# Kernel tuning notes

Measured on AMD Instinct MI355X. Metric: run time of the kernel, lower is better.

## Reference

```python
import jax, jax.numpy as jnp
import numpy as np

N_NODES = 50000
N_EDGES = 400000
HID = 256
NUM_LAYERS = 2
NUM_LEVELS = 8  # depth of the constructed leveled DAG


def _build_dag_edges():
    # Leveled DAG: NUM_LEVELS levels of equal size; every edge goes from
    # level l (src) to level l+1 (dst), guaranteeing termination in
    # exactly NUM_LEVELS topological sweeps.
    rng = np.random.default_rng(0)
    per_level = N_NODES // NUM_LEVELS
    dst_level = rng.integers(1, NUM_LEVELS, size=N_EDGES)
    dst = dst_level * per_level + rng.integers(0, per_level, size=N_EDGES)
    src = (dst_level - 1) * per_level + rng.integers(0, per_level, size=N_EDGES)
    return jnp.asarray(np.stack([src, dst]).astype(np.int32))


def setup_inputs() -> dict:
    key = jax.random.key(0)
    ks = jax.random.split(key, 8)
    s = 0.05
    V = jax.random.normal(ks[0], (N_NODES, HID), dtype=jnp.float32)
    E = _build_dag_edges()
    dense_w = jax.random.normal(ks[1], (HID, HID), dtype=jnp.float32) * s
    dense_b = jax.random.normal(ks[2], (HID,), dtype=jnp.float32) * s
    gru_w_ih = jax.random.normal(ks[3], (NUM_LAYERS, 3 * HID, HID), dtype=jnp.float32) * s
    gru_w_hh = jax.random.normal(ks[4], (NUM_LAYERS, 3 * HID, HID), dtype=jnp.float32) * s
    gru_b_ih = jax.random.normal(ks[5], (NUM_LAYERS, 3 * HID), dtype=jnp.float32) * s
    gru_b_hh = jax.random.normal(ks[6], (NUM_LAYERS, 3 * HID), dtype=jnp.float32) * s
    return {"V": V, "E": E, "dense_w": dense_w, "dense_b": dense_b,
            "gru_w_ih": gru_w_ih, "gru_w_hh": gru_w_hh,
            "gru_b_ih": gru_b_ih, "gru_b_hh": gru_b_hh}


def _gru_cell(x, h, w_ih, w_hh, b_ih, b_hh):
    gi = x @ w_ih.T + b_ih
    gh = h @ w_hh.T + b_hh
    i_r, i_z, i_n = jnp.split(gi, 3, axis=-1)
    h_r, h_z, h_n = jnp.split(gh, 3, axis=-1)
    r = jax.nn.sigmoid(i_r + h_r)
    z = jax.nn.sigmoid(i_z + h_z)
    n = jnp.tanh(i_n + r * h_n)
    return (1.0 - z) * n + z * h


def _dag_gru_layer(x, src, dst, w_ih, w_hh, b_ih, b_hh):
    N = x.shape[0]
    H = w_hh.shape[1]

    def step(carry, _):
        hidden, avail = carry
        # nodes that are dst of an edge whose source is still available
        blocked = jnp.zeros((N,), dtype=bool).at[dst].max(avail[src])
        leaf = avail & ~blocked
        use = leaf[dst]  # edges feeding a leaf node this sweep
        msgs = jnp.where(use[:, None], hidden[src], 0.0)  # [E, H]
        agg = jax.ops.segment_sum(msgs, dst, num_segments=N)  # [N, H]
        new_h = _gru_cell(x, agg, w_ih, w_hh, b_ih, b_hh)
        hidden = jnp.where(leaf[:, None], new_h, hidden)
        return (hidden, avail & ~leaf), None

    init = (jnp.zeros((N, H), dtype=x.dtype), jnp.ones((N,), dtype=bool))
    (hidden, _), _ = jax.lax.scan(step, init, None, length=NUM_LEVELS)
    return hidden


def reference(V, E, dense_w, dense_b, gru_w_ih, gru_w_hh, gru_b_ih, gru_b_hh):
    src, dst = E[0], E[1]
    hidden = V @ dense_w.T + dense_b
    for l in range(NUM_LAYERS):
        hidden = _dag_gru_layer(hidden, src, dst,
                                gru_w_ih[l], gru_w_hh[l],
                                gru_b_ih[l], gru_b_hh[l])
    return hidden
```

## Files before the change

kernel.cpp:

```cpp
#include <hip/hip_runtime.h>

#define HID 256
#define NSTEPS 8

typedef __attribute__((ext_vector_type(4))) float f32x4;
typedef __attribute__((ext_vector_type(8))) short s16x8;

__device__ __forceinline__ unsigned short f2bf(float f) {
  unsigned u = __builtin_bit_cast(unsigned, f);
  u += 0x7fffu + ((u >> 16) & 1u);
  return (unsigned short)(u >> 16);
}
__device__ __forceinline__ float bf2f(unsigned short s) {
  return __builtin_bit_cast(float, ((unsigned)s) << 16);
}

__device__ __forceinline__ f32x4 mfma16(s16x8 a, s16x8 b, f32x4 c) {
  return __builtin_amdgcn_mfma_f32_16x16x32_bf16(a, b, c, 0, 0, 0);
}

__device__ __forceinline__ void split3(const float* p, s16x8& a0, s16x8& a1, s16x8& a2) {
  f32x4 u = *(const f32x4*)p;
  f32x4 v = *(const f32x4*)(p + 4);
  float f[8] = {u[0], u[1], u[2], u[3], v[0], v[1], v[2], v[3]};
#pragma unroll
  for (int j = 0; j < 8; ++j) {
    unsigned short l0 = f2bf(f[j]);
    float r1 = f[j] - bf2f(l0);
    unsigned short l1 = f2bf(r1);
    float r2 = r1 - bf2f(l1);
    a0[j] = (short)l0;
    a1[j] = (short)l1;
    a2[j] = (short)f2bf(r2);
  }
}


__global__ void k_limb(const float* __restrict__ in, short* __restrict__ o0,
                       short* __restrict__ o1, short* __restrict__ o2, int n) {
  int i = blockIdx.x * 256 + threadIdx.x;
  if (i < n) {
    float x = in[i];
    unsigned short l0 = f2bf(x);
    float r1 = x - bf2f(l0);
    unsigned short l1 = f2bf(r1);
    o0[i] = (short)l0;
    o1[i] = (short)l1;
    o2[i] = (short)f2bf(r1 - bf2f(l1));
  }
}


__global__ void k_indeg(const int* __restrict__ dst, int* __restrict__ indeg, int E) {
  int e = blockIdx.x * blockDim.x + threadIdx.x;
  if (e < E) atomicAdd(&indeg[dst[e]], 1);
}

__global__ void k_blocksum(const int* __restrict__ indeg, int* __restrict__ bsum, int N) {
  __shared__ int s[256];
  int i = blockIdx.x * 256 + threadIdx.x;
  s[threadIdx.x] = (i < N) ? indeg[i] : 0;
  __syncthreads();
  for (int st = 128; st > 0; st >>= 1) {
    if (threadIdx.x < st) s[threadIdx.x] += s[threadIdx.x + st];
    __syncthreads();
  }
  if (threadIdx.x == 0) bsum[blockIdx.x] = s[0];
}

__global__ void k_bscan(const int* __restrict__ bsum, int* __restrict__ boff,
                        int NB, int* __restrict__ total) {
  if (threadIdx.x == 0 && blockIdx.x == 0) {
    int a = 0;
    for (int i = 0; i < NB; ++i) { boff[i] = a; a += bsum[i]; }
    *total = a;
  }
}

__global__ void k_scan3(const int* __restrict__ indeg, const int* __restrict__ boff,
                        int* __restrict__ csr_off, int N) {
  __shared__ int s[256];
  int tx = threadIdx.x;
  int i = blockIdx.x * 256 + tx;
  int v = (i < N) ? indeg[i] : 0;
  s[tx] = v;
  __syncthreads();
  for (int st = 1; st < 256; st <<= 1) {
    int t = (tx >= st) ? s[tx - st] : 0;
    __syncthreads();
    s[tx] += t;
    __syncthreads();
  }
  if (i < N) csr_off[i] = boff[blockIdx.x] + s[tx] - v;
}

__global__ void k_fill(const int* __restrict__ src, const int* __restrict__ dst,
                       const int* __restrict__ csr_off, int* __restrict__ cursor,
                       int* __restrict__ csr_src, int E) {
  int e = blockIdx.x * blockDim.x + threadIdx.x;
  if (e < E) {
    int d = dst[e];
    int p = atomicAdd(&cursor[d], 1);
    csr_src[csr_off[d] + p] = src[e];
  }
}


__global__ void k_aggf(const float* __restrict__ H, int s, int PB,
                       const int* __restrict__ csr_off, const int* __restrict__ csr_src,
                       float* __restrict__ aggF, short* __restrict__ G0,
                       short* __restrict__ G1, short* __restrict__ G2) {
  int c = threadIdx.x;
  for (int r = blockIdx.x; r < PB; r += gridDim.x) {
    int node = s * PB + r;
    int b = csr_off[node], e = csr_off[node + 1];
    float acc = 0.f;
    for (int j = b; j < e; ++j) acc += H[(size_t)csr_src[j] * HID + c];
    size_t o = (size_t)r * HID + c;
    aggF[o] = acc;
    unsigned short l0 = f2bf(acc);
    float r1 = acc - bf2f(l0);
    unsigned short l1 = f2bf(r1);
    G0[o] = (short)l0;
    G1[o] = (short)l1;
    G2[o] = (short)f2bf(r1 - bf2f(l1));
  }
}

__global__ __launch_bounds__(256, 2)
void k_dense8(const float* __restrict__ V, const short* __restrict__ dwS,
              const float* __restrict__ db,
              short* __restrict__ A0, short* __restrict__ A1,
              short* __restrict__ A2, int M) {
  __shared__ s16x8 lds[2][24 * 64];
  const int tid = threadIdx.x;
  const int w = tid >> 6, lane = tid & 63;
  const int lr = lane & 15, lg = lane >> 4;
  const int c0 = blockIdx.x * 128;
  const int m0 = blockIdx.y * 64 + w * 16;
  const float* xrow = V + (size_t)min(m0 + lr, M - 1) * HID;

  const short* sp[6];
  int so[6];
#pragma unroll
  for (int q = 0; q < 6; ++q) {
    int f = w * 6 + q;
    int a = f >> 3, t = f & 7;
    sp[q] = dwS + a * (HID * HID) + (size_t)(c0 + t * 16 + lr) * HID + lg * 8;
    so[q] = f * 64 + lane;
  }

  s16x8 rr[6];
#pragma unroll
  for (int q = 0; q < 6; ++q) rr[q] = *(const s16x8*)(sp[q]);
#pragma unroll
  for (int q = 0; q < 6; ++q) lds[0][so[q]] = rr[q];

  f32x4 acc[8];
#pragma unroll
  for (int t = 0; t < 8; ++t) acc[t] = (f32x4){0.f, 0.f, 0.f, 0.f};

  for (int kc = 0; kc < 8; ++kc) {
    if (kc < 7) {
#pragma unroll
      for (int q = 0; q < 6; ++q) rr[q] = *(const s16x8*)(sp[q] + (kc + 1) * 32);
    }
    __syncthreads();
    const s16x8* buf = lds[kc & 1];
    int kb = kc * 32 + lg * 8;
    s16x8 x0, x1, x2;
    split3(xrow + kb, x0, x1, x2);
#pragma unroll
    for (int t = 0; t < 8; ++t) {
      s16x8 w0f = buf[(0 * 8 + t) * 64 + lane];
      s16x8 w1f = buf[(1 * 8 + t) * 64 + lane];
      s16x8 w2f = buf[(2 * 8 + t) * 64 + lane];
      f32x4 a = acc[t];
      a = mfma16(x0, w0f, a);
      a = mfma16(x0, w1f, a);
      a = mfma16(x1, w0f, a);
      a = mfma16(x1, w1f, a);
      a = mfma16(x0, w2f, a);
      a = mfma16(x2, w0f, a);
      acc[t] = a;
    }
    if (kc < 7) {
#pragma unroll
      for (int q = 0; q < 6; ++q) lds[(kc + 1) & 1][so[q]] = rr[q];
    }
  }

#pragma unroll
  for (int t = 0; t < 8; ++t) {
    int col = c0 + t * 16 + lr;
    float bb = db[col];
#pragma unroll
    for (int r = 0; r < 4; ++r) {
      int row = m0 + lg * 4 + r;
      if (row < M) {
        float v = acc[t][r] + bb;
        unsigned short l0 = f2bf(v);
        float r1 = v - bf2f(l0);
        unsigned short l1 = f2bf(r1);
        size_t o = (size_t)row * HID + col;
        A0[o] = (short)l0;
        A1[o] = (short)l1;
        A2[o] = (short)f2bf(r1 - bf2f(l1));
      }
    }
  }
}

template<bool OUTL>
__global__ __launch_bounds__(256, 2)
void k_step8(const short* __restrict__ X0, const short* __restrict__ X1,
             const short* __restrict__ X2,
             const short* __restrict__ G0, const short* __restrict__ G1,
             const short* __restrict__ G2,
             const float* __restrict__ aggF,
             const short* __restrict__ wSL,
             const float* __restrict__ bi, const float* __restrict__ bh,
             int s, int PB, float* __restrict__ Hf,
             short* __restrict__ L0, short* __restrict__ L1, short* __restrict__ L2) {
  __shared__ s16x8 lds[2][36 * 64];
  const int tid = threadIdx.x;
  const int w = tid >> 6, lane = tid & 63;
  const int lr = lane & 15, lg = lane >> 4;
  const int c0 = blockIdx.x * 32;
  const int m0w = blockIdx.y * 128 + w * 32;
  const int nb = s * PB;
  const int AS = 768 * HID;

  const short* sp[9];
  int so[9];
#pragma unroll
  for (int q = 0; q < 9; ++q) {
    int f = w * 9 + q;
    int a = f / 6, gt = f - a * 6, g = gt >> 1, t = gt & 1;
    sp[q] = wSL + (size_t)a * AS + (size_t)(g * HID + c0 + t * 16 + lr) * HID + lg * 8;
    so[q] = f * 64 + lane;
  }

  s16x8 rr[9];
#pragma unroll
  for (int q = 0; q < 9; ++q) rr[q] = *(const s16x8*)(sp[q]);
#pragma unroll
  for (int q = 0; q < 9; ++q) lds[0][so[q]] = rr[q];

  f32x4 acci[3][2][2], acch[3][2][2];
#pragma unroll
  for (int g = 0; g < 3; ++g)
#pragma unroll
    for (int t = 0; t < 2; ++t)
#pragma unroll
      for (int rg = 0; rg < 2; ++rg) {
        acci[g][t][rg] = (f32x4){0.f, 0.f, 0.f, 0.f};
        acch[g][t][rg] = (f32x4){0.f, 0.f, 0.f, 0.f};
      }

  int rowA[2];
  rowA[0] = min(m0w + lr, PB - 1);
  rowA[1] = min(m0w + 16 + lr, PB - 1);

  for (int kc = 0; kc < 8; ++kc) {
    if (kc < 7) {
#pragma unroll
      for (int q = 0; q < 9; ++q) rr[q] = *(const s16x8*)(sp[q] + (kc + 1) * 32);
    }
    __syncthreads();
    const s16x8* buf = lds[kc & 1];
    const int kb = kc * 32 + lg * 8;
    s16x8 x0[2], x1[2], x2[2], g0[2], g1[2], g2[2];
#pragma unroll
    for (int rg = 0; rg < 2; ++rg) {
      size_t xb = (size_t)(nb + rowA[rg]) * HID + kb;
      x0[rg] = *(const s16x8*)&X0[xb];
      x1[rg] = *(const s16x8*)&X1[xb];
      x2[rg] = *(const s16x8*)&X2[xb];
      size_t gb = (size_t)rowA[rg] * HID + kb;
      g0[rg] = *(const s16x8*)&G0[gb];
      g1[rg] = *(const s16x8*)&G1[gb];
      g2[rg] = *(const s16x8*)&G2[gb];
    }
#pragma unroll
    for (int g = 0; g < 3; ++g) {
#pragma unroll
      for (int t = 0; t < 2; ++t) {
        s16x8 wi0f = buf[(0 * 6 + g * 2 + t) * 64 + lane];
        s16x8 wi1f = buf[(1 * 6 + g * 2 + t) * 64 + lane];
        s16x8 wi2f = buf[(2 * 6 + g * 2 + t) * 64 + lane];
        s16x8 wh0f = buf[(3 * 6 + g * 2 + t) * 64 + lane];
        s16x8 wh1f = buf[(4 * 6 + g * 2 + t) * 64 + lane];
        s16x8 wh2f = buf[(5 * 6 + g * 2 + t) * 64 + lane];
#pragma unroll
        for (int rg = 0; rg < 2; ++rg) {
          f32x4 a = acci[g][t][rg];
          a = mfma16(x0[rg], wi0f, a);
          a = mfma16(x0[rg], wi1f, a);
          a = mfma16(x1[rg], wi0f, a);
          a = mfma16(x1[rg], wi1f, a);
          a = mfma16(x0[rg], wi2f, a);
          a = mfma16(x2[rg], wi0f, a);
          acci[g][t][rg] = a;
          f32x4 h = acch[g][t][rg];
          h = mfma16(g0[rg], wh0f, h);
          h = mfma16(g0[rg], wh1f, h);
          h = mfma16(g1[rg], wh0f, h);
          h = mfma16(g1[rg], wh1f, h);
          h = mfma16(g0[rg], wh2f, h);
          h = mfma16(g2[rg], wh0f, h);
          acch[g][t][rg] = h;
        }
      }
    }
    if (kc < 7) {
#pragma unroll
      for (int q = 0; q < 9; ++q) lds[(kc + 1) & 1][so[q]] = rr[q];
    }
  }

#pragma unroll
  for (int t = 0; t < 2; ++t) {
    int col = c0 + t * 16 + lr;
    float bir = bi[col], biz = bi[HID + col], bin = bi[2 * HID + col];
    float bhr = bh[col], bhz = bh[HID + col], bhn = bh[2 * HID + col];
#pragma unroll
    for (int rg = 0; rg < 2; ++rg) {
#pragma unroll
      for (int r = 0; r < 4; ++r) {
        int row = m0w + rg * 16 + lg * 4 + r;
        if (row < PB) {
          float ir = acci[0][t][rg][r] + bir;
          float iz = acci[1][t][rg][r] + biz;
          float in_ = acci[2][t][rg][r] + bin;
          float hr = acch[0][t][rg][r] + bhr;
          float hz = acch[1][t][rg][r] + bhz;
          float hn = acch[2][t][rg][r] + bhn;
          float rgate = 1.f / (1.f + expf(-(ir + hr)));
          float zg = 1.f / (1.f + expf(-(iz + hz)));
          float ng = tanhf(in_ + rgate * hn);
          float a = aggF[(size_t)row * HID + col];
          float h = (1.f - zg) * ng + zg * a;
          size_t o = (size_t)(nb + row) * HID + col;
          Hf[o] = h;
          if (OUTL) {
            unsigned short l0 = f2bf(h);
            float r1 = h - bf2f(l0);
            unsigned short l1 = f2bf(r1);
            L0[o] = (short)l0;
            L1[o] = (short)l1;
            L2[o] = (short)f2bf(r1 - bf2f(l1));
          }
        }
      }
    }
  }
}


extern "C" void kernel_launch(void* const* d_in, const int* in_sizes, int n_in,
                              void* d_out, int out_size, void* d_ws, size_t ws_size,
                              hipStream_t stream) {
  const float* V = (const float*)d_in[0];
  const int* E = (const int*)d_in[1];
  const float* dense_w = (const float*)d_in[2];
  const float* dense_b = (const float*)d_in[3];
  const float* w_ih = (const float*)d_in[4];
  const float* w_hh = (const float*)d_in[5];
  const float* b_ih = (const float*)d_in[6];
  const float* b_hh = (const float*)d_in[7];
  const int N = in_sizes[0] / HID;
  const int Ecnt = in_sizes[1] / 2;
  const int PB = N / NSTEPS;
  const int* src = E;
  const int* dst = E + Ecnt;
  float* out = (float*)d_out;

  const size_t AS = (size_t)768 * HID;

  char* p = (char*)d_ws;
  short* A0 = (short*)p;   p += (size_t)N * HID * 2;
  short* A1 = (short*)p;   p += (size_t)N * HID * 2;
  short* A2 = (short*)p;   p += (size_t)N * HID * 2;
  float* B = (float*)p;    p += (size_t)N * HID * 4;
  short* B0 = (short*)p;   p += (size_t)N * HID * 2;
  short* B1 = (short*)p;   p += (size_t)N * HID * 2;
  short* B2 = (short*)p;   p += (size_t)N * HID * 2;
  float* aggF = (float*)p; p += (size_t)PB * HID * 4;
  short* G0 = (short*)p;   p += (size_t)PB * HID * 2;
  short* G1 = (short*)p;   p += (size_t)PB * HID * 2;
  short* G2 = (short*)p;   p += (size_t)PB * HID * 2;
  short* dwS = (short*)p;  p += (size_t)3 * HID * HID * 2;
  short* wS = (short*)p;   p += (size_t)2 * 6 * AS * 2;
  int* indeg = (int*)p;    p += (size_t)N * 4;
  int* cursor = (int*)p;   p += (size_t)N * 4;
  int* csr_off = (int*)p;  p += (size_t)(N + 1) * 4;
  int* csr_src = (int*)p;  p += (size_t)Ecnt * 4;
  int* bsum = (int*)p;     p += 256 * 4;
  int* boff = (int*)p;     p += 256 * 4;

  hipMemsetAsync(indeg, 0, (size_t)2 * N * 4, stream);

  const int TB = 256;
  const int egrid = (Ecnt + TB - 1) / TB;
  const int NB = (N + 255) / 256;
  const int wgrid = ((int)AS + 255) / 256;

  k_limb<<<(HID * HID + 255) / 256, TB, 0, stream>>>(
      dense_w, dwS, dwS + HID * HID, dwS + 2 * HID * HID, HID * HID);
  for (int l = 0; l < 2; ++l) {
    k_limb<<<wgrid, TB, 0, stream>>>(w_ih + l * AS, wS + (l * 6 + 0) * AS,
                                     wS + (l * 6 + 1) * AS, wS + (l * 6 + 2) * AS, (int)AS);
    k_limb<<<wgrid, TB, 0, stream>>>(w_hh + l * AS, wS + (l * 6 + 3) * AS,
                                     wS + (l * 6 + 4) * AS, wS + (l * 6 + 5) * AS, (int)AS);
  }

  k_dense8<<<dim3(2, (N + 63) / 64), TB, 0, stream>>>(V, dwS, dense_b, A0, A1, A2, N);

  k_indeg<<<egrid, TB, 0, stream>>>(dst, indeg, Ecnt);
  k_blocksum<<<NB, TB, 0, stream>>>(indeg, bsum, N);
  k_bscan<<<1, 1, 0, stream>>>(bsum, boff, NB, csr_off + N);
  k_scan3<<<NB, TB, 0, stream>>>(indeg, boff, csr_off, N);
  k_fill<<<egrid, TB, 0, stream>>>(src, dst, csr_off, cursor, csr_src, Ecnt);

  const dim3 sgrid(HID / 32, (PB + 127) / 128);

  for (int s = 0; s < NSTEPS; ++s) {
    k_aggf<<<2048, TB, 0, stream>>>(B, s, PB, csr_off, csr_src, aggF, G0, G1, G2);
    k_step8<true><<<sgrid, TB, 0, stream>>>(A0, A1, A2, G0, G1, G2, aggF,
                                            wS, b_ih, b_hh, s, PB, B, B0, B1, B2);
  }
  for (int s = 0; s < NSTEPS; ++s) {
    k_aggf<<<2048, TB, 0, stream>>>(out, s, PB, csr_off, csr_src, aggF, G0, G1, G2);
    k_step8<false><<<sgrid, TB, 0, stream>>>(B0, B1, B2, G0, G1, G2, aggF,
                                             wS + 6 * AS, b_ih + 768, b_hh + 768, s, PB,
                                             out, nullptr, nullptr, nullptr);
  }
}
```

Baseline: 1.492 ms.

## Pipeline both GRU layers across levels in shared launches and vectorize aggregation

Runs layer 0 at level t and layer 1 at level t-1 within the same launch via a z grid dimension, halving the number of sequential aggregation/step launches and doubling per-launch parallelism. Aggregation is rewritten to use one wavefront per node with float4 loads instead of one 256-thread block per node. Adds duplicated aggregate buffers and per-block pointer selection; correctness relies on the layer-1 dependency being satisfied by the previous launch.

```diff
diff --git a/kernel.cpp b/kernel.cpp
--- a/kernel.cpp
+++ b/kernel.cpp
@@ -5,6 +5,7 @@
 
 typedef __attribute__((ext_vector_type(4))) float f32x4;
 typedef __attribute__((ext_vector_type(8))) short s16x8;
+typedef __attribute__((ext_vector_type(4))) short s16x4;
 
 __device__ __forceinline__ unsigned short f2bf(float f) {
   unsigned u = __builtin_bit_cast(unsigned, f);
@@ -106,25 +107,49 @@
 }
 
 
-__global__ void k_aggf(const float* __restrict__ H, int s, int PB,
-                       const int* __restrict__ csr_off, const int* __restrict__ csr_src,
-                       float* __restrict__ aggF, short* __restrict__ G0,
-                       short* __restrict__ G1, short* __restrict__ G2) {
-  int c = threadIdx.x;
-  for (int r = blockIdx.x; r < PB; r += gridDim.x) {
-    int node = s * PB + r;
-    int b = csr_off[node], e = csr_off[node + 1];
-    float acc = 0.f;
-    for (int j = b; j < e; ++j) acc += H[(size_t)csr_src[j] * HID + c];
-    size_t o = (size_t)r * HID + c;
-    aggF[o] = acc;
-    unsigned short l0 = f2bf(acc);
-    float r1 = acc - bf2f(l0);
+__global__ void k_aggf2(const float* __restrict__ HA, const float* __restrict__ HB,
+                        int t, int PB,
+                        const int* __restrict__ csr_off, const int* __restrict__ csr_src,
+                        float* __restrict__ aggFA, float* __restrict__ aggFB,
+                        short* __restrict__ GA0, short* __restrict__ GA1,
+                        short* __restrict__ GA2,
+                        short* __restrict__ GB0, short* __restrict__ GB1,
+                        short* __restrict__ GB2) {
+  const int z = blockIdx.z;
+  const int s = t - z;
+  if (s < 0 || s >= NSTEPS) return;
+  const float* H = z ? HB : HA;
+  float* aggF = z ? aggFB : aggFA;
+  short* G0 = z ? GB0 : GA0;
+  short* G1 = z ? GB1 : GA1;
+  short* G2 = z ? GB2 : GA2;
+
+  const int grp = threadIdx.x >> 6, lane = threadIdx.x & 63;
+  const int r = blockIdx.x * 4 + grp;
+  if (r >= PB) return;
+  const int node = s * PB + r;
+  const int b = csr_off[node], e = csr_off[node + 1];
+  const int c4 = lane * 4;
+  f32x4 acc = (f32x4){0.f, 0.f, 0.f, 0.f};
+  for (int j = b; j < e; ++j) {
+    f32x4 v = *(const f32x4*)&H[(size_t)csr_src[j] * HID + c4];
+    acc[0] += v[0]; acc[1] += v[1]; acc[2] += v[2]; acc[3] += v[3];
+  }
+  size_t o = (size_t)r * HID + c4;
+  *(f32x4*)&aggF[o] = acc;
+  s16x4 g0, g1, g2;
+#pragma unroll
+  for (int q = 0; q < 4; ++q) {
+    unsigned short l0 = f2bf(acc[q]);
+    float r1 = acc[q] - bf2f(l0);
     unsigned short l1 = f2bf(r1);
-    G0[o] = (short)l0;
-    G1[o] = (short)l1;
-    G2[o] = (short)f2bf(r1 - bf2f(l1));
-  }
+    g0[q] = (short)l0;
+    g1[q] = (short)l1;
+    g2[q] = (short)f2bf(r1 - bf2f(l1));
+  }
+  *(s16x4*)&G0[o] = g0;
+  *(s16x4*)&G1[o] = g1;
+  *(s16x4*)&G2[o] = g2;
 }
 
 __global__ __launch_bounds__(256, 2)
@@ -211,17 +236,37 @@
   }
 }
 
-template<bool OUTL>
 __global__ __launch_bounds__(256, 2)
-void k_step8(const short* __restrict__ X0, const short* __restrict__ X1,
-             const short* __restrict__ X2,
-             const short* __restrict__ G0, const short* __restrict__ G1,
-             const short* __restrict__ G2,
-             const float* __restrict__ aggF,
-             const short* __restrict__ wSL,
-             const float* __restrict__ bi, const float* __restrict__ bh,
-             int s, int PB, float* __restrict__ Hf,
-             short* __restrict__ L0, short* __restrict__ L1, short* __restrict__ L2) {
+void k_step2(const short* __restrict__ A0, const short* __restrict__ A1,
+             const short* __restrict__ A2,
+             const short* __restrict__ B0, const short* __restrict__ B1,
+             const short* __restrict__ B2,
+             const short* __restrict__ GA0, const short* __restrict__ GA1,
+             const short* __restrict__ GA2,
+             const short* __restrict__ GB0, const short* __restrict__ GB1,
+             const short* __restrict__ GB2,
+             const float* __restrict__ aggFA, const float* __restrict__ aggFB,
+             const short* __restrict__ wS,
+             const float* __restrict__ b_ih, const float* __restrict__ b_hh,
+             int t, int PB, float* __restrict__ Bfp, float* __restrict__ outp) {
+  const int z = blockIdx.z;
+  const int s = t - z;
+  if (s < 0 || s >= NSTEPS) return;
+
+  const short* X0 = z ? B0 : A0;
+  const short* X1 = z ? B1 : A1;
+  const short* X2 = z ? B2 : A2;
+  const short* G0 = z ? GB0 : GA0;
+  const short* G1 = z ? GB1 : GA1;
+  const short* G2 = z ? GB2 : GA2;
+  const float* aggF = z ? aggFB : aggFA;
+  const int AS = 768 * HID;
+  const short* wSL = wS + (size_t)z * 6 * AS;
+  const float* bi = b_ih + z * 768;
+  const float* bh = b_hh + z * 768;
+  float* Hf = z ? outp : Bfp;
+  const bool outl = (z == 0);
+
   __shared__ s16x8 lds[2][36 * 64];
   const int tid = threadIdx.x;
   const int w = tid >> 6, lane = tid & 63;
@@ -229,15 +274,14 @@
   const int c0 = blockIdx.x * 32;
   const int m0w = blockIdx.y * 128 + w * 32;
   const int nb = s * PB;
-  const int AS = 768 * HID;
 
   const short* sp[9];
   int so[9];
 #pragma unroll
   for (int q = 0; q < 9; ++q) {
     int f = w * 9 + q;
-    int a = f / 6, gt = f - a * 6, g = gt >> 1, t = gt & 1;
-    sp[q] = wSL + (size_t)a * AS + (size_t)(g * HID + c0 + t * 16 + lr) * HID + lg * 8;
+    int a = f / 6, gt = f - a * 6, g = gt >> 1, tt = gt & 1;
+    sp[q] = wSL + (size_t)a * AS + (size_t)(g * HID + c0 + tt * 16 + lr) * HID + lg * 8;
     so[q] = f * 64 + lane;
   }
 
@@ -251,11 +295,11 @@
 #pragma unroll
   for (int g = 0; g < 3; ++g)
 #pragma unroll
-    for (int t = 0; t < 2; ++t)
+    for (int tt = 0; tt < 2; ++tt)
 #pragma unroll
       for (int rg = 0; rg < 2; ++rg) {
-        acci[g][t][rg] = (f32x4){0.f, 0.f, 0.f, 0.f};
-        acch[g][t][rg] = (f32x4){0.f, 0.f, 0.f, 0.f};
+        acci[g][tt][rg] = (f32x4){0.f, 0.f, 0.f, 0.f};
+        acch[g][tt][rg] = (f32x4){0.f, 0.f, 0.f, 0.f};
       }
 
   int rowA[2];
@@ -285,31 +329,31 @@
 #pragma unroll
     for (int g = 0; g < 3; ++g) {
 #pragma unroll
-      for (int t = 0; t < 2; ++t) {
-        s16x8 wi0f = buf[(0 * 6 + g * 2 + t) * 64 + lane];
-        s16x8 wi1f = buf[(1 * 6 + g * 2 + t) * 64 + lane];
-        s16x8 wi2f = buf[(2 * 6 + g * 2 + t) * 64 + lane];
-        s16x8 wh0f = buf[(3 * 6 + g * 2 + t) * 64 + lane];
-        s16x8 wh1f = buf[(4 * 6 + g * 2 + t) * 64 + lane];
-        s16x8 wh2f = buf[(5 * 6 + g * 2 + t) * 64 + lane];
+      for (int tt = 0; tt < 2; ++tt) {
+        s16x8 wi0f = buf[(0 * 6 + g * 2 + tt) * 64 + lane];
+        s16x8 wi1f = buf[(1 * 6 + g * 2 + tt) * 64 + lane];
+        s16x8 wi2f = buf[(2 * 6 + g * 2 + tt) * 64 + lane];
+        s16x8 wh0f = buf[(3 * 6 + g * 2 + tt) * 64 + lane];
+        s16x8 wh1f = buf[(4 * 6 + g * 2 + tt) * 64 + lane];
+        s16x8 wh2f = buf[(5 * 6 + g * 2 + tt) * 64 + lane];
 #pragma unroll
         for (int rg = 0; rg < 2; ++rg) {
-          f32x4 a = acci[g][t][rg];
+          f32x4 a = acci[g][tt][rg];
           a = mfma16(x0[rg], wi0f, a);
           a = mfma16(x0[rg], wi1f, a);
           a = mfma16(x1[rg], wi0f, a);
           a = mfma16(x1[rg], wi1f, a);
           a = mfma16(x0[rg], wi2f, a);
           a = mfma16(x2[rg], wi0f, a);
-          acci[g][t][rg] = a;
-          f32x4 h = acch[g][t][rg];
+          acci[g][tt][rg] = a;
+          f32x4 h = acch[g][tt][rg];
           h = mfma16(g0[rg], wh0f, h);
           h = mfma16(g0[rg], wh1f, h);
           h = mfma16(g1[rg], wh0f, h);
           h = mfma16(g1[rg], wh1f, h);
           h = mfma16(g0[rg], wh2f, h);
           h = mfma16(g2[rg], wh0f, h);
-          acch[g][t][rg] = h;
+          acch[g][tt][rg] = h;
         }
       }
     }
@@ -320,8 +364,8 @@
   }
 
 #pragma unroll
-  for (int t = 0; t < 2; ++t) {
-    int col = c0 + t * 16 + lr;
+  for (int tt = 0; tt < 2; ++tt) {
+    int col = c0 + tt * 16 + lr;
     float bir = bi[col], biz = bi[HID + col], bin = bi[2 * HID + col];
     float bhr = bh[col], bhz = bh[HID + col], bhn = bh[2 * HID + col];
 #pragma unroll
@@ -330,12 +374,12 @@
       for (int r = 0; r < 4; ++r) {
         int row = m0w + rg * 16 + lg * 4 + r;
         if (row < PB) {
-          float ir = acci[0][t][rg][r] + bir;
-          float iz = acci[1][t][rg][r] + biz;
-          float in_ = acci[2][t][rg][r] + bin;
-          float hr = acch[0][t][rg][r] + bhr;
-          float hz = acch[1][t][rg][r] + bhz;
-          float hn = acch[2][t][rg][r] + bhn;
+          float ir = acci[0][tt][rg][r] + bir;
+          float iz = acci[1][tt][rg][r] + biz;
+          float in_ = acci[2][tt][rg][r] + bin;
+          float hr = acch[0][tt][rg][r] + bhr;
+          float hz = acch[1][tt][rg][r] + bhz;
+          float hn = acch[2][tt][rg][r] + bhn;
           float rgate = 1.f / (1.f + expf(-(ir + hr)));
           float zg = 1.f / (1.f + expf(-(iz + hz)));
           float ng = tanhf(in_ + rgate * hn);
@@ -343,13 +387,13 @@
           float h = (1.f - zg) * ng + zg * a;
           size_t o = (size_t)(nb + row) * HID + col;
           Hf[o] = h;
-          if (OUTL) {
+          if (outl) {
             unsigned short l0 = f2bf(h);
             float r1 = h - bf2f(l0);
             unsigned short l1 = f2bf(r1);
-            L0[o] = (short)l0;
-            L1[o] = (short)l1;
-            L2[o] = (short)f2bf(r1 - bf2f(l1));
+            ((short*)B0)[o] = (short)l0;
+            ((short*)B1)[o] = (short)l1;
+            ((short*)B2)[o] = (short)f2bf(r1 - bf2f(l1));
           }
         }
       }
@@ -379,25 +423,29 @@
   const size_t AS = (size_t)768 * HID;
 
   char* p = (char*)d_ws;
-  short* A0 = (short*)p;   p += (size_t)N * HID * 2;
-  short* A1 = (short*)p;   p += (size_t)N * HID * 2;
-  short* A2 = (short*)p;   p += (size_t)N * HID * 2;
-  float* B = (float*)p;    p += (size_t)N * HID * 4;
-  short* B0 = (short*)p;   p += (size_t)N * HID * 2;
-  short* B1 = (short*)p;   p += (size_t)N * HID * 2;
-  short* B2 = (short*)p;   p += (size_t)N * HID * 2;
-  float* aggF = (float*)p; p += (size_t)PB * HID * 4;
-  short* G0 = (short*)p;   p += (size_t)PB * HID * 2;
-  short* G1 = (short*)p;   p += (size_t)PB * HID * 2;
-  short* G2 = (short*)p;   p += (size_t)PB * HID * 2;
-  short* dwS = (short*)p;  p += (size_t)3 * HID * HID * 2;
-  short* wS = (short*)p;   p += (size_t)2 * 6 * AS * 2;
-  int* indeg = (int*)p;    p += (size_t)N * 4;
-  int* cursor = (int*)p;   p += (size_t)N * 4;
-  int* csr_off = (int*)p;  p += (size_t)(N + 1) * 4;
-  int* csr_src = (int*)p;  p += (size_t)Ecnt * 4;
-  int* bsum = (int*)p;     p += 256 * 4;
-  int* boff = (int*)p;     p += 256 * 4;
+  short* A0 = (short*)p;    p += (size_t)N * HID * 2;
+  short* A1 = (short*)p;    p += (size_t)N * HID * 2;
+  short* A2 = (short*)p;    p += (size_t)N * HID * 2;
+  float* B = (float*)p;     p += (size_t)N * HID * 4;
+  short* B0 = (short*)p;    p += (size_t)N * HID * 2;
+  short* B1 = (short*)p;    p += (size_t)N * HID * 2;
+  short* B2 = (short*)p;    p += (size_t)N * HID * 2;
+  float* aggFA = (float*)p; p += (size_t)PB * HID * 4;
+  float* aggFB = (float*)p; p += (size_t)PB * HID * 4;
+  short* GA0 = (short*)p;   p += (size_t)PB * HID * 2;
+  short* GA1 = (short*)p;   p += (size_t)PB * HID * 2;
+  short* GA2 = (short*)p;   p += (size_t)PB * HID * 2;
+  short* GB0 = (short*)p;   p += (size_t)PB * HID * 2;
+  short* GB1 = (short*)p;   p += (size_t)PB * HID * 2;
+  short* GB2 = (short*)p;   p += (size_t)PB * HID * 2;
+  short* dwS = (short*)p;   p += (size_t)3 * HID * HID * 2;
+  short* wS = (short*)p;    p += (size_t)2 * 6 * AS * 2;
+  int* indeg = (int*)p;     p += (size_t)N * 4;
+  int* cursor = (int*)p;    p += (size_t)N * 4;
+  int* csr_off = (int*)p;   p += (size_t)(N + 1) * 4;
+  int* csr_src = (int*)p;   p += (size_t)Ecnt * 4;
+  int* bsum = (int*)p;      p += 256 * 4;
+  int* boff = (int*)p;      p += 256 * 4;
 
   hipMemsetAsync(indeg, 0, (size_t)2 * N * 4, stream);
 
@@ -423,17 +471,14 @@
   k_scan3<<<NB, TB, 0, stream>>>(indeg, boff, csr_off, N);
   k_fill<<<egrid, TB, 0, stream>>>(src, dst, csr_off, cursor, csr_src, Ecnt);
 
-  const dim3 sgrid(HID / 32, (PB + 127) / 128);
-
-  for (int s = 0; s < NSTEPS; ++s) {
-    k_aggf<<<2048, TB, 0, stream>>>(B, s, PB, csr_off, csr_src, aggF, G0, G1, G2);
-    k_step8<true><<<sgrid, TB, 0, stream>>>(A0, A1, A2, G0, G1, G2, aggF,
-                                            wS, b_ih, b_hh, s, PB, B, B0, B1, B2);
-  }
-  for (int s = 0; s < NSTEPS; ++s) {
-    k_aggf<<<2048, TB, 0, stream>>>(out, s, PB, csr_off, csr_src, aggF, G0, G1, G2);
-    k_step8<false><<<sgrid, TB, 0, stream>>>(B0, B1, B2, G0, G1, G2, aggF,
-                                             wS + 6 * AS, b_ih + 768, b_hh + 768, s, PB,
-                                             out, nullptr, nullptr, nullptr);
-  }
-}
+  const dim3 agrid((PB + 3) / 4, 1, 2);
+  const dim3 sgrid(HID / 32, (PB + 127) / 128, 2);
+  for (int t = 0; t <= NSTEPS; ++t) {
+    k_aggf2<<<agrid, TB, 0, stream>>>(B, out, t, PB, csr_off, csr_src,
+                                      aggFA, aggFB, GA0, GA1, GA2, GB0, GB1, GB2);
+    k_step2<<<sgrid, TB, 0, stream>>>(A0, A1, A2, B0, B1, B2,
+                                      GA0, GA1, GA2, GB0, GB1, GB2,
+                                      aggFA, aggFB, wS, b_ih, b_hh,
+                                      t, PB, B, out);
+  }
+}
```

After: 1.358 ms. 9.0% less time.
